# Kernel optimization log

Measured on AMD Instinct MI355X. Metric: run time of the kernel, lower is better.

The kernel has to match this reference:

```python
import jax, jax.numpy as jnp
import numpy as np

N, E, F_IN, H, OUT, G = 40000, 640000, 128, 128, 10, 256


def setup_inputs() -> dict:
    key = jax.random.key(0)
    ks = jax.random.split(key, 8)
    x = jax.random.normal(ks[0], (N, F_IN), dtype=jnp.float32)
    edge_index = jax.random.randint(ks[1], (2, E), 0, N, dtype=jnp.int32)
    batch = jnp.sort(jax.random.randint(ks[2], (N,), 0, G, dtype=jnp.int32))
    W1 = jax.random.normal(ks[3], (F_IN, H), dtype=jnp.float32) / np.sqrt(F_IN)
    b1 = jnp.zeros((H,), dtype=jnp.float32)
    W2 = jax.random.normal(ks[4], (H, H), dtype=jnp.float32) / np.sqrt(H)
    b2 = jnp.zeros((H,), dtype=jnp.float32)
    Wfc = jax.random.normal(ks[5], (H, OUT), dtype=jnp.float32) / np.sqrt(H)
    bfc = jnp.zeros((OUT,), dtype=jnp.float32)
    return {"x": x, "edge_index": edge_index, "batch": batch,
            "W1": W1, "b1": b1, "W2": W2, "b2": b2, "Wfc": Wfc, "bfc": bfc}


def _gcn_conv(x, W, b, row, col, num_nodes):
    # x' = D^{-1/2} (A+I) D^{-1/2} (x W) + b   (self-loops already in row/col)
    xw = x @ W                                            # [N, H]
    ones = jnp.ones(row.shape[0], dtype=x.dtype)
    deg = jax.ops.segment_sum(ones, col, num_segments=num_nodes)
    dinv = jnp.where(deg > 0, jax.lax.rsqrt(jnp.maximum(deg, 1.0)), 0.0)
    norm = dinv[row] * dinv[col]                          # [E+N]
    msg = xw[row] * norm[:, None]                         # gather + scale
    return jax.ops.segment_sum(msg, col, num_segments=num_nodes) + b


def reference(x, edge_index, batch, W1, b1, W2, b2, Wfc, bfc):
    num_nodes = x.shape[0]
    loop = jnp.arange(num_nodes, dtype=edge_index.dtype)
    row = jnp.concatenate([edge_index[0], loop])
    col = jnp.concatenate([edge_index[1], loop])

    h = jax.nn.relu(_gcn_conv(x, W1, b1, row, col, num_nodes))
    h = jax.nn.relu(_gcn_conv(h, W2, b2, row, col, num_nodes))

    # global_mean_pool over graph ids
    sums = jax.ops.segment_sum(h, batch, num_segments=G)  # [G, H]
    cnt = jax.ops.segment_sum(jnp.ones(num_nodes, h.dtype), batch, num_segments=G)
    pooled = sums / jnp.maximum(cnt, 1.0)[:, None]

    logits = pooled @ Wfc + bfc                           # [G, OUT]
    return jax.nn.log_softmax(logits, axis=-1)
```

## Files before the change

### kernel.cpp

```cpp
#include <hip/hip_runtime.h>
#include <math.h>

#define H_DIM 128
#define OUT_DIM 10

typedef __attribute__((ext_vector_type(8))) __bf16 bf16x8;
typedef __attribute__((ext_vector_type(8))) unsigned short ushort8;
typedef __attribute__((ext_vector_type(4))) float f32x4;

__device__ inline unsigned short f2bf_rne(float f) {
    unsigned int u = __float_as_uint(f);
    unsigned int r = u + 0x7FFFu + ((u >> 16) & 1u);
    return (unsigned short)(r >> 16);
}
__device__ inline float bf_lo(unsigned int u) { return __uint_as_float(u << 16); }
__device__ inline float bf_hi(unsigned int u) { return __uint_as_float(u & 0xFFFF0000u); }

__global__ __launch_bounds__(256) void prep_kernel(const float* __restrict__ W1,
                                                   const float* __restrict__ W2,
                                                   unsigned short* __restrict__ Wt1Hi,
                                                   unsigned short* __restrict__ Wt1Lo,
                                                   unsigned short* __restrict__ Wt2Hi,
                                                   unsigned short* __restrict__ Wt2Lo,
                                                   const float* __restrict__ X,
                                                   unsigned short* __restrict__ Xhi,
                                                   unsigned short* __restrict__ Xlo,
                                                   int total8, int hb,
                                                   const int* __restrict__ col,
                                                   int* __restrict__ cnt,
                                                   int* __restrict__ rank, int E) {
    if (blockIdx.x < hb) {
        int e = blockIdx.x * 256 + threadIdx.x;
        if (e < E) rank[e] = atomicAdd(&cnt[col[e]], 1);
    } else if (blockIdx.x < hb + 128) {
        int i = (blockIdx.x - hb) * 256 + threadIdx.x;
        const float* src   = (i < 16384) ? W1    : W2;
        unsigned short* dh = (i < 16384) ? Wt1Hi : Wt2Hi;
        unsigned short* dl = (i < 16384) ? Wt1Lo : Wt2Lo;
        int idx = i & 16383;
        int k = idx >> 7, n = idx & 127;
        float v = src[idx];
        unsigned short hbv = f2bf_rne(v);
        float hf = __uint_as_float((unsigned int)hbv << 16);
        unsigned short lb = f2bf_rne(v - hf);
        dh[n * H_DIM + k] = hbv;
        dl[n * H_DIM + k] = lb;
    } else {
        int i = (blockIdx.x - hb - 128) * 256 + threadIdx.x;
        if (i >= total8) return;
        const float* p = X + (size_t)i * 8;
        f32x4 a = *(const f32x4*)p;
        f32x4 b = *(const f32x4*)(p + 4);
        float v[8] = {a.x, a.y, a.z, a.w, b.x, b.y, b.z, b.w};
        ushort8 h, l;
        #pragma unroll
        for (int j = 0; j < 8; ++j) {
            unsigned short hbv = f2bf_rne(v[j]);
            float hf = __uint_as_float((unsigned int)hbv << 16);
            h[j] = hbv;
            l[j] = f2bf_rne(v[j] - hf);
        }
        *(ushort8*)(Xhi + (size_t)i * 8) = h;
        *(ushort8*)(Xlo + (size_t)i * 8) = l;
    }
}

__global__ __launch_bounds__(256) void scan_phase1(const int* __restrict__ cnt,
                                                   int* __restrict__ blockSums,
                                                   float* __restrict__ dinv, int N) {
    __shared__ int red[256];
    int base = blockIdx.x * 1024;
    int t = threadIdx.x;
    int s = 0;
    for (int i = 0; i < 4; ++i) {
        int idx = base + t * 4 + i;
        if (idx < N) {
            int cv = cnt[idx];
            s += cv;
            dinv[idx] = rsqrtf((float)cv + 1.0f);
        }
    }
    red[t] = s;
    __syncthreads();
    for (int d = 128; d > 0; d >>= 1) {
        if (t < d) red[t] += red[t + d];
        __syncthreads();
    }
    if (t == 0) blockSums[blockIdx.x] = red[0];
}

__global__ __launch_bounds__(256) void scan_phase23(const int* __restrict__ cnt,
                                                    const int* __restrict__ blockSums,
                                                    int* __restrict__ offs, int N, int B) {
    __shared__ int red[256];
    __shared__ int bsum[256];
    int base = blockIdx.x * 1024;
    int t = threadIdx.x;

    bsum[t] = (t < B && t < (int)blockIdx.x) ? blockSums[t] : 0;

    int v[4];
    int s = 0;
    for (int i = 0; i < 4; ++i) {
        int idx = base + t * 4 + i;
        v[i] = (idx < N) ? cnt[idx] : 0;
        s += v[i];
    }
    red[t] = s;
    __syncthreads();
    for (int d = 128; d > 0; d >>= 1) {
        if (t < d) bsum[t] += bsum[t + d];
        __syncthreads();
    }
    for (int d = 1; d < 256; d <<= 1) {
        int x = (t >= d) ? red[t - d] : 0;
        __syncthreads();
        red[t] += x;
        __syncthreads();
    }
    int run = bsum[0] + ((t == 0) ? 0 : red[t - 1]);
    for (int i = 0; i < 4; ++i) {
        int idx = base + t * 4 + i;
        if (idx < N) { offs[idx] = run; run += v[i]; }
    }
    if ((int)blockIdx.x == B - 1 && t == 255) offs[N] = run;
}

__global__ __launch_bounds__(256) void scatter_gemm1(
        const int* __restrict__ row, const int* __restrict__ col,
        const int* __restrict__ rank, const float* __restrict__ dinv,
        const int* __restrict__ offs, int2* __restrict__ csr, int E, int sb,
        const unsigned short* __restrict__ Ahi, const unsigned short* __restrict__ Alo,
        const unsigned short* __restrict__ WtHi, const unsigned short* __restrict__ WtLo,
        unsigned short* __restrict__ Yb, int N) {
    if (blockIdx.x < (unsigned)sb) {
        int e = blockIdx.x * 256 + threadIdx.x;
        if (e >= E) return;
        int r = row[e], c = col[e], rk = rank[e];
        int pos = offs[c] + rk;
        int2 p; p.x = r; p.y = __float_as_int(dinv[r] * dinv[c]);
        csr[pos] = p;
        return;
    }
    int blk  = blockIdx.x - sb;
    int lane = threadIdx.x & 63;
    int wv   = threadIdx.x >> 6;
    int m16  = lane & 15;
    int quad = lane >> 4;
    int nodeBase = blk * 32;

    f32x4 acc[2][2] = {};

    #pragma unroll
    for (int kt = 0; kt < 4; ++kt) {
        int k0 = kt * 32 + quad * 8;

        ushort8 aHi[2], aLo[2];
        #pragma unroll
        for (int mi = 0; mi < 2; ++mi) {
            int node = nodeBase + mi * 16 + m16;
            if (node >= N) node = N - 1;
            size_t off = (size_t)node * H_DIM + k0;
            aHi[mi] = *(const ushort8*)(Ahi + off);
            aLo[mi] = *(const ushort8*)(Alo + off);
        }

        ushort8 bHi[2], bLo[2];
        #pragma unroll
        for (int ni = 0; ni < 2; ++ni) {
            int n = (wv * 2 + ni) * 16 + m16;
            size_t off = (size_t)n * H_DIM + k0;
            bHi[ni] = *(const ushort8*)(WtHi + off);
            bLo[ni] = *(const ushort8*)(WtLo + off);
        }

        #pragma unroll
        for (int mi = 0; mi < 2; ++mi)
            #pragma unroll
            for (int ni = 0; ni < 2; ++ni) {
                acc[mi][ni] = __builtin_amdgcn_mfma_f32_16x16x32_bf16(
                    __builtin_bit_cast(bf16x8, aHi[mi]),
                    __builtin_bit_cast(bf16x8, bHi[ni]), acc[mi][ni], 0, 0, 0);
                acc[mi][ni] = __builtin_amdgcn_mfma_f32_16x16x32_bf16(
                    __builtin_bit_cast(bf16x8, aLo[mi]),
                    __builtin_bit_cast(bf16x8, bHi[ni]), acc[mi][ni], 0, 0, 0);
                acc[mi][ni] = __builtin_amdgcn_mfma_f32_16x16x32_bf16(
                    __builtin_bit_cast(bf16x8, aHi[mi]),
                    __builtin_bit_cast(bf16x8, bLo[ni]), acc[mi][ni], 0, 0, 0);
            }
    }

    #pragma unroll
    for (int mi = 0; mi < 2; ++mi)
        #pragma unroll
        for (int r = 0; r < 4; ++r) {
            int node = nodeBase + mi * 16 + quad * 4 + r;
            if (node < N) {
                #pragma unroll
                for (int ni = 0; ni < 2; ++ni) {
                    int c = (wv * 2 + ni) * 16 + m16;
                    Yb[(size_t)node * H_DIM + c] = f2bf_rne(acc[mi][ni][r]);
                }
            }
        }
}

__global__ __launch_bounds__(256) void gemm_mfma_bf16A(const unsigned short* __restrict__ Xb,
                                                       const unsigned short* __restrict__ WtHi,
                                                       const unsigned short* __restrict__ WtLo,
                                                       unsigned short* __restrict__ Yb, int N) {
    int lane = threadIdx.x & 63;
    int wv   = threadIdx.x >> 6;
    int m16  = lane & 15;
    int quad = lane >> 4;
    int nodeBase = blockIdx.x * 32;

    f32x4 acc[2][2] = {};

    #pragma unroll
    for (int kt = 0; kt < 4; ++kt) {
        int k0 = kt * 32 + quad * 8;

        ushort8 a[2];
        #pragma unroll
        for (int mi = 0; mi < 2; ++mi) {
            int node = nodeBase + mi * 16 + m16;
            if (node >= N) node = N - 1;
            a[mi] = *(const ushort8*)(Xb + (size_t)node * H_DIM + k0);
        }

        ushort8 bHi[2], bLo[2];
        #pragma unroll
        for (int ni = 0; ni < 2; ++ni) {
            int n = (wv * 2 + ni) * 16 + m16;
            size_t off = (size_t)n * H_DIM + k0;
            bHi[ni] = *(const ushort8*)(WtHi + off);
            bLo[ni] = *(const ushort8*)(WtLo + off);
        }

        #pragma unroll
        for (int mi = 0; mi < 2; ++mi)
            #pragma unroll
            for (int ni = 0; ni < 2; ++ni) {
                acc[mi][ni] = __builtin_amdgcn_mfma_f32_16x16x32_bf16(
                    __builtin_bit_cast(bf16x8, a[mi]),
                    __builtin_bit_cast(bf16x8, bHi[ni]), acc[mi][ni], 0, 0, 0);
                acc[mi][ni] = __builtin_amdgcn_mfma_f32_16x16x32_bf16(
                    __builtin_bit_cast(bf16x8, a[mi]),
                    __builtin_bit_cast(bf16x8, bLo[ni]), acc[mi][ni], 0, 0, 0);
            }
    }

    #pragma unroll
    for (int mi = 0; mi < 2; ++mi)
        #pragma unroll
        for (int r = 0; r < 4; ++r) {
            int node = nodeBase + mi * 16 + quad * 4 + r;
            if (node < N) {
                #pragma unroll
                for (int ni = 0; ni < 2; ++ni) {
                    int c = (wv * 2 + ni) * 16 + m16;
                    Yb[(size_t)node * H_DIM + c] = f2bf_rne(acc[mi][ni][r]);
                }
            }
        }
}

__global__ __launch_bounds__(256) void agg_fused(const unsigned short* __restrict__ XWb,
                                                 const float* __restrict__ dinv,
                                                 const int2* __restrict__ csr,
                                                 const int* __restrict__ offs,
                                                 const float* __restrict__ bias,
                                                 unsigned short* __restrict__ OUTb, int N) {
    int wave = (blockIdx.x * 256 + threadIdx.x) >> 6;
    int lane = threadIdx.x & 63;
    if (wave >= N) return;
    int c = wave;
    int start = offs[c], end = offs[c + 1];
    float dc = dinv[c];
    const unsigned int* XW32 = (const unsigned int*)XWb;

    float ax0, ay0;
    {
        unsigned int u = XW32[(size_t)c * 64 + lane];
        float s = dc * dc;
        ax0 = bf_lo(u) * s; ay0 = bf_hi(u) * s;
    }
    float ax1 = 0.f, ay1 = 0.f, ax2 = 0.f, ay2 = 0.f, ax3 = 0.f, ay3 = 0.f;

    for (int base = start; base < end; base += 64) {
        int m = end - base; if (m > 64) m = 64;
        int2 ce; ce.x = 0; ce.y = 0;
        if (lane < m) ce = csr[base + lane];

        int j = 0;
        for (; j + 3 < m; j += 4) {
            int r0 = __shfl(ce.x, j);     int b0 = __shfl(ce.y, j);
            int r1 = __shfl(ce.x, j + 1); int b1 = __shfl(ce.y, j + 1);
            int r2 = __shfl(ce.x, j + 2); int b2 = __shfl(ce.y, j + 2);
            int r3 = __shfl(ce.x, j + 3); int b3 = __shfl(ce.y, j + 3);
            unsigned int g0 = XW32[(size_t)r0 * 64 + lane];
            unsigned int g1 = XW32[(size_t)r1 * 64 + lane];
            unsigned int g2 = XW32[(size_t)r2 * 64 + lane];
            unsigned int g3 = XW32[(size_t)r3 * 64 + lane];
            float n0 = __int_as_float(b0);
            float n1 = __int_as_float(b1);
            float n2 = __int_as_float(b2);
            float n3 = __int_as_float(b3);
            ax0 += bf_lo(g0) * n0; ay0 += bf_hi(g0) * n0;
            ax1 += bf_lo(g1) * n1; ay1 += bf_hi(g1) * n1;
            ax2 += bf_lo(g2) * n2; ay2 += bf_hi(g2) * n2;
            ax3 += bf_lo(g3) * n3; ay3 += bf_hi(g3) * n3;
        }
        for (; j < m; ++j) {
            int r = __shfl(ce.x, j); int b = __shfl(ce.y, j);
            unsigned int g = XW32[(size_t)r * 64 + lane];
            float nrm = __int_as_float(b);
            ax1 += bf_lo(g) * nrm; ay1 += bf_hi(g) * nrm;
        }
    }
    float ax = (ax0 + ax1) + (ax2 + ax3);
    float ay = (ay0 + ay1) + (ay2 + ay3);
    float2 b = ((const float2*)bias)[lane];
    ax = fmaxf(ax + b.x, 0.f);
    ay = fmaxf(ay + b.y, 0.f);
    unsigned int o = (unsigned int)f2bf_rne(ax) | ((unsigned int)f2bf_rne(ay) << 16);
    ((unsigned int*)(OUTb + (size_t)c * H_DIM))[lane] = o;
}

__global__ __launch_bounds__(256) void pool_partial(const unsigned short* __restrict__ Hb,
                                                    const int* __restrict__ batch,
                                                    float* __restrict__ pooledSum, int N) {
    __shared__ int sb[64];
    int base = blockIdx.x * 64;
    int t = threadIdx.x;
    if (t < 64) {
        int idx = base + t;
        sb[t] = (idx < N) ? batch[idx] : -1;
    }
    __syncthreads();
    int f   = t & 127;
    int sub = t >> 7;
    int n0  = sub * 32;
    float acc = 0.f;
    int curg = -1;
    #pragma unroll 4
    for (int i = 0; i < 32; ++i) {
        int n = base + n0 + i;
        if (n >= N) break;
        int g = sb[n0 + i];
        if (g != curg) {
            if (curg >= 0) atomicAdd(&pooledSum[curg * H_DIM + f], acc);
            acc = 0.f; curg = g;
        }
        acc += __uint_as_float(((unsigned int)Hb[(size_t)n * H_DIM + f]) << 16);
    }
    if (curg >= 0) atomicAdd(&pooledSum[curg * H_DIM + f], acc);
}

__global__ __launch_bounds__(64) void head_kernel(const float* __restrict__ pooledSum,
                                                  const int* __restrict__ batch,
                                                  const float* __restrict__ Wfc,
                                                  const float* __restrict__ bfc,
                                                  float* __restrict__ out, int N) {
    __shared__ float sl[OUT_DIM + 2];
    __shared__ int bounds[2];
    int g = blockIdx.x;
    int j = threadIdx.x;
    if (j < 2) {
        int v = g + j;
        int lo = 0, hi = N;
        while (lo < hi) {
            int mid = (lo + hi) >> 1;
            if (batch[mid] < v) lo = mid + 1; else hi = mid;
        }
        bounds[j] = lo;
    }
    __syncthreads();
    int cnt = bounds[1] - bounds[0];
    float inv = 1.0f / (float)(cnt > 0 ? cnt : 1);
    if (j < OUT_DIM) {
        float acc = 0.f;
        const float* p = pooledSum + g * H_DIM;
        for (int k = 0; k < H_DIM; ++k) acc += p[k] * Wfc[k * OUT_DIM + j];
        sl[j] = acc * inv + bfc[j];
    }
    __syncthreads();
    if (j == 0) {
        float m = sl[0];
        for (int i = 1; i < OUT_DIM; ++i) m = fmaxf(m, sl[i]);
        float s = 0.f;
        for (int i = 0; i < OUT_DIM; ++i) s += expf(sl[i] - m);
        sl[OUT_DIM] = m + logf(s);
    }
    __syncthreads();
    if (j < OUT_DIM) out[g * OUT_DIM + j] = sl[j] - sl[OUT_DIM];
}

extern "C" void kernel_launch(void* const* d_in, const int* in_sizes, int n_in,
                              void* d_out, int out_size, void* d_ws, size_t ws_size,
                              hipStream_t stream) {
    const float* x     = (const float*)d_in[0];
    const int*   ei    = (const int*)  d_in[1];
    const int*   batch = (const int*)  d_in[2];
    const float* W1    = (const float*)d_in[3];
    const float* b1    = (const float*)d_in[4];
    const float* W2    = (const float*)d_in[5];
    const float* b2    = (const float*)d_in[6];
    const float* Wfc   = (const float*)d_in[7];
    const float* bfc   = (const float*)d_in[8];
    float* out = (float*)d_out;

    int N = in_sizes[2];
    int E = in_sizes[1] / 2;
    int G = out_size / OUT_DIM;
    const int* row = ei;
    const int* col = ei + E;

    char* wsb = (char*)d_ws;
    size_t nAlign = (size_t)((N + 256) / 256) * 256;
    size_t eAlign = (size_t)((E + 255) / 256) * 256;
    int*   cnt       = (int*)wsb;
    float* pooledSum = (float*)(cnt + nAlign);
    int*   offs      = (int*)(pooledSum + (size_t)G * H_DIM);
    int*   rank      = offs + nAlign;
    float* dinv      = (float*)(rank + eAlign);
    int2*  csr       = (int2*)(dinv + nAlign);
    unsigned short* Xb = (unsigned short*)(csr + E);
    unsigned short* Hb = Xb + (size_t)N * H_DIM;
    int* blockSums = (int*)(Hb + (size_t)N * H_DIM);
    unsigned short* Wt1Hi = (unsigned short*)(blockSums + 256);
    unsigned short* Wt1Lo = Wt1Hi + H_DIM * H_DIM;
    unsigned short* Wt2Hi = Wt1Lo + H_DIM * H_DIM;
    unsigned short* Wt2Lo = Wt2Hi + H_DIM * H_DIM;
    unsigned short* Xhi = Wt2Lo + H_DIM * H_DIM;
    unsigned short* Xlo = Xhi + (size_t)N * H_DIM;

    int scanBlocks = (N + 1023) / 1024;
    int total8 = N * H_DIM / 8;
    int xb = (total8 + 255) / 256;
    int histBlocks = (E + 255) / 256;
    int gemmBlocks = (N + 31) / 32;

    hipMemsetAsync(cnt, 0, (nAlign + (size_t)G * H_DIM) * sizeof(int), stream);

    prep_kernel<<<histBlocks + 128 + xb, 256, 0, stream>>>(
        W1, W2, Wt1Hi, Wt1Lo, Wt2Hi, Wt2Lo, x, Xhi, Xlo, total8, histBlocks,
        col, cnt, rank, E);

    scan_phase1<<<scanBlocks, 256, 0, stream>>>(cnt, blockSums, dinv, N);
    scan_phase23<<<scanBlocks, 256, 0, stream>>>(cnt, blockSums, offs, N, scanBlocks);

    scatter_gemm1<<<histBlocks + gemmBlocks, 256, 0, stream>>>(
        row, col, rank, dinv, offs, csr, E, histBlocks,
        Xhi, Xlo, Wt1Hi, Wt1Lo, Xb, N);

    int aggBlocks = (N + 3) / 4;

    agg_fused<<<aggBlocks, 256, 0, stream>>>(Xb, dinv, csr, offs, b1, Hb, N);

    gemm_mfma_bf16A<<<gemmBlocks, 256, 0, stream>>>(Hb, Wt2Hi, Wt2Lo, Xb, N);
    agg_fused<<<aggBlocks, 256, 0, stream>>>(Xb, dinv, csr, offs, b2, Hb, N);

    pool_partial<<<(N + 63) / 64, 256, 0, stream>>>(Hb, batch, pooledSum, N);
    head_kernel<<<G, 64, 0, stream>>>(pooledSum, batch, Wfc, bfc, out, N);
}
```

Before: 249.2 us.

## Fuse X bf16 split into GEMM1 and mean-pool into second aggregation

The input features are no longer pre-split into hi/lo bf16 buffers in the prep kernel. GEMM1 now reads fp32 X directly and does the split in registers, which removes a full write and re-read of two N×128 bf16 arrays. The second aggregation is templated to reduce its four per-wave node outputs in shared memory and atomically add them into the pooled sums, so the separate pool kernel and the Hb write/read are gone. In exchange it adds a block barrier and more atomics (up to four per feature per block) in the aggregation, and GEMM1 reads fp32 with redundant conversions across waves.

```diff
diff --git a/kernel.cpp b/kernel.cpp
--- a/kernel.cpp
+++ b/kernel.cpp
@@ -22,17 +22,14 @@
                                                    unsigned short* __restrict__ Wt1Lo,
                                                    unsigned short* __restrict__ Wt2Hi,
                                                    unsigned short* __restrict__ Wt2Lo,
-                                                   const float* __restrict__ X,
-                                                   unsigned short* __restrict__ Xhi,
-                                                   unsigned short* __restrict__ Xlo,
-                                                   int total8, int hb,
+                                                   int hb,
                                                    const int* __restrict__ col,
                                                    int* __restrict__ cnt,
                                                    int* __restrict__ rank, int E) {
-    if (blockIdx.x < hb) {
+    if (blockIdx.x < (unsigned)hb) {
         int e = blockIdx.x * 256 + threadIdx.x;
         if (e < E) rank[e] = atomicAdd(&cnt[col[e]], 1);
-    } else if (blockIdx.x < hb + 128) {
+    } else {
         int i = (blockIdx.x - hb) * 256 + threadIdx.x;
         const float* src   = (i < 16384) ? W1    : W2;
         unsigned short* dh = (i < 16384) ? Wt1Hi : Wt2Hi;
@@ -45,23 +42,6 @@
         unsigned short lb = f2bf_rne(v - hf);
         dh[n * H_DIM + k] = hbv;
         dl[n * H_DIM + k] = lb;
-    } else {
-        int i = (blockIdx.x - hb - 128) * 256 + threadIdx.x;
-        if (i >= total8) return;
-        const float* p = X + (size_t)i * 8;
-        f32x4 a = *(const f32x4*)p;
-        f32x4 b = *(const f32x4*)(p + 4);
-        float v[8] = {a.x, a.y, a.z, a.w, b.x, b.y, b.z, b.w};
-        ushort8 h, l;
-        #pragma unroll
-        for (int j = 0; j < 8; ++j) {
-            unsigned short hbv = f2bf_rne(v[j]);
-            float hf = __uint_as_float((unsigned int)hbv << 16);
-            h[j] = hbv;
-            l[j] = f2bf_rne(v[j] - hf);
-        }
-        *(ushort8*)(Xhi + (size_t)i * 8) = h;
-        *(ushort8*)(Xlo + (size_t)i * 8) = l;
     }
 }
 
@@ -130,7 +110,7 @@
         const int* __restrict__ row, const int* __restrict__ col,
         const int* __restrict__ rank, const float* __restrict__ dinv,
         const int* __restrict__ offs, int2* __restrict__ csr, int E, int sb,
-        const unsigned short* __restrict__ Ahi, const unsigned short* __restrict__ Alo,
+        const float* __restrict__ Xf,
         const unsigned short* __restrict__ WtHi, const unsigned short* __restrict__ WtLo,
         unsigned short* __restrict__ Yb, int N) {
     if (blockIdx.x < (unsigned)sb) {
@@ -160,9 +140,16 @@
         for (int mi = 0; mi < 2; ++mi) {
             int node = nodeBase + mi * 16 + m16;
             if (node >= N) node = N - 1;
-            size_t off = (size_t)node * H_DIM + k0;
-            aHi[mi] = *(const ushort8*)(Ahi + off);
-            aLo[mi] = *(const ushort8*)(Alo + off);
+            const float* p = Xf + (size_t)node * H_DIM + k0;
+            f32x4 u = *(const f32x4*)p;
+            f32x4 w = *(const f32x4*)(p + 4);
+            float vv[8] = {u.x, u.y, u.z, u.w, w.x, w.y, w.z, w.w};
+            #pragma unroll
+            for (int j = 0; j < 8; ++j) {
+                unsigned short hbv = f2bf_rne(vv[j]);
+                aHi[mi][j] = hbv;
+                aLo[mi][j] = f2bf_rne(vv[j] - __uint_as_float((unsigned int)hbv << 16));
+            }
         }
 
         ushort8 bHi[2], bLo[2];
@@ -266,96 +253,101 @@
         }
 }
 
-__global__ __launch_bounds__(256) void agg_fused(const unsigned short* __restrict__ XWb,
-                                                 const float* __restrict__ dinv,
-                                                 const int2* __restrict__ csr,
-                                                 const int* __restrict__ offs,
-                                                 const float* __restrict__ bias,
-                                                 unsigned short* __restrict__ OUTb, int N) {
+template <int POOL>
+__global__ __launch_bounds__(256) void agg_fused_t(const unsigned short* __restrict__ XWb,
+                                                   const float* __restrict__ dinv,
+                                                   const int2* __restrict__ csr,
+                                                   const int* __restrict__ offs,
+                                                   const float* __restrict__ bias,
+                                                   unsigned short* __restrict__ OUTb,
+                                                   const int* __restrict__ batch,
+                                                   float* __restrict__ pooledSum, int N) {
     int wave = (blockIdx.x * 256 + threadIdx.x) >> 6;
     int lane = threadIdx.x & 63;
-    if (wave >= N) return;
+    int wv   = threadIdx.x >> 6;
+    bool active = wave < N;
+    if (!POOL && !active) return;
+
+    float ax = 0.f, ay = 0.f;
     int c = wave;
-    int start = offs[c], end = offs[c + 1];
-    float dc = dinv[c];
-    const unsigned int* XW32 = (const unsigned int*)XWb;
-
-    float ax0, ay0;
-    {
-        unsigned int u = XW32[(size_t)c * 64 + lane];
-        float s = dc * dc;
-        ax0 = bf_lo(u) * s; ay0 = bf_hi(u) * s;
-    }
-    float ax1 = 0.f, ay1 = 0.f, ax2 = 0.f, ay2 = 0.f, ax3 = 0.f, ay3 = 0.f;
-
-    for (int base = start; base < end; base += 64) {
-        int m = end - base; if (m > 64) m = 64;
-        int2 ce; ce.x = 0; ce.y = 0;
-        if (lane < m) ce = csr[base + lane];
-
-        int j = 0;
-        for (; j + 3 < m; j += 4) {
-            int r0 = __shfl(ce.x, j);     int b0 = __shfl(ce.y, j);
-            int r1 = __shfl(ce.x, j + 1); int b1 = __shfl(ce.y, j + 1);
-            int r2 = __shfl(ce.x, j + 2); int b2 = __shfl(ce.y, j + 2);
-            int r3 = __shfl(ce.x, j + 3); int b3 = __shfl(ce.y, j + 3);
-            unsigned int g0 = XW32[(size_t)r0 * 64 + lane];
-            unsigned int g1 = XW32[(size_t)r1 * 64 + lane];
-            unsigned int g2 = XW32[(size_t)r2 * 64 + lane];
-            unsigned int g3 = XW32[(size_t)r3 * 64 + lane];
-            float n0 = __int_as_float(b0);
-            float n1 = __int_as_float(b1);
-            float n2 = __int_as_float(b2);
-            float n3 = __int_as_float(b3);
-            ax0 += bf_lo(g0) * n0; ay0 += bf_hi(g0) * n0;
-            ax1 += bf_lo(g1) * n1; ay1 += bf_hi(g1) * n1;
-            ax2 += bf_lo(g2) * n2; ay2 += bf_hi(g2) * n2;
-            ax3 += bf_lo(g3) * n3; ay3 += bf_hi(g3) * n3;
-        }
-        for (; j < m; ++j) {
-            int r = __shfl(ce.x, j); int b = __shfl(ce.y, j);
-            unsigned int g = XW32[(size_t)r * 64 + lane];
-            float nrm = __int_as_float(b);
-            ax1 += bf_lo(g) * nrm; ay1 += bf_hi(g) * nrm;
-        }
-    }
-    float ax = (ax0 + ax1) + (ax2 + ax3);
-    float ay = (ay0 + ay1) + (ay2 + ay3);
-    float2 b = ((const float2*)bias)[lane];
-    ax = fmaxf(ax + b.x, 0.f);
-    ay = fmaxf(ay + b.y, 0.f);
-    unsigned int o = (unsigned int)f2bf_rne(ax) | ((unsigned int)f2bf_rne(ay) << 16);
-    ((unsigned int*)(OUTb + (size_t)c * H_DIM))[lane] = o;
-}
-
-__global__ __launch_bounds__(256) void pool_partial(const unsigned short* __restrict__ Hb,
-                                                    const int* __restrict__ batch,
-                                                    float* __restrict__ pooledSum, int N) {
-    __shared__ int sb[64];
-    int base = blockIdx.x * 64;
-    int t = threadIdx.x;
-    if (t < 64) {
-        int idx = base + t;
-        sb[t] = (idx < N) ? batch[idx] : -1;
-    }
-    __syncthreads();
-    int f   = t & 127;
-    int sub = t >> 7;
-    int n0  = sub * 32;
-    float acc = 0.f;
-    int curg = -1;
-    #pragma unroll 4
-    for (int i = 0; i < 32; ++i) {
-        int n = base + n0 + i;
-        if (n >= N) break;
-        int g = sb[n0 + i];
-        if (g != curg) {
-            if (curg >= 0) atomicAdd(&pooledSum[curg * H_DIM + f], acc);
-            acc = 0.f; curg = g;
-        }
-        acc += __uint_as_float(((unsigned int)Hb[(size_t)n * H_DIM + f]) << 16);
-    }
-    if (curg >= 0) atomicAdd(&pooledSum[curg * H_DIM + f], acc);
+    if (active) {
+        int start = offs[c], end = offs[c + 1];
+        float dc = dinv[c];
+        const unsigned int* XW32 = (const unsigned int*)XWb;
+
+        float ax0, ay0;
+        {
+            unsigned int u = XW32[(size_t)c * 64 + lane];
+            float s = dc * dc;
+            ax0 = bf_lo(u) * s; ay0 = bf_hi(u) * s;
+        }
+        float ax1 = 0.f, ay1 = 0.f, ax2 = 0.f, ay2 = 0.f, ax3 = 0.f, ay3 = 0.f;
+
+        for (int base = start; base < end; base += 64) {
+            int m = end - base; if (m > 64) m = 64;
+            int2 ce; ce.x = 0; ce.y = 0;
+            if (lane < m) ce = csr[base + lane];
+
+            int j = 0;
+            for (; j + 3 < m; j += 4) {
+                int r0 = __shfl(ce.x, j);     int b0 = __shfl(ce.y, j);
+                int r1 = __shfl(ce.x, j + 1); int b1 = __shfl(ce.y, j + 1);
+                int r2 = __shfl(ce.x, j + 2); int b2 = __shfl(ce.y, j + 2);
+                int r3 = __shfl(ce.x, j + 3); int b3 = __shfl(ce.y, j + 3);
+                unsigned int g0 = XW32[(size_t)r0 * 64 + lane];
+                unsigned int g1 = XW32[(size_t)r1 * 64 + lane];
+                unsigned int g2 = XW32[(size_t)r2 * 64 + lane];
+                unsigned int g3 = XW32[(size_t)r3 * 64 + lane];
+                float n0 = __int_as_float(b0);
+                float n1 = __int_as_float(b1);
+                float n2 = __int_as_float(b2);
+                float n3 = __int_as_float(b3);
+                ax0 += bf_lo(g0) * n0; ay0 += bf_hi(g0) * n0;
+                ax1 += bf_lo(g1) * n1; ay1 += bf_hi(g1) * n1;
+                ax2 += bf_lo(g2) * n2; ay2 += bf_hi(g2) * n2;
+                ax3 += bf_lo(g3) * n3; ay3 += bf_hi(g3) * n3;
+            }
+            for (; j < m; ++j) {
+                int r = __shfl(ce.x, j); int b = __shfl(ce.y, j);
+                unsigned int g = XW32[(size_t)r * 64 + lane];
+                float nrm = __int_as_float(b);
+                ax1 += bf_lo(g) * nrm; ay1 += bf_hi(g) * nrm;
+            }
+        }
+        ax = (ax0 + ax1) + (ax2 + ax3);
+        ay = (ay0 + ay1) + (ay2 + ay3);
+        float2 b = ((const float2*)bias)[lane];
+        ax = fmaxf(ax + b.x, 0.f);
+        ay = fmaxf(ay + b.y, 0.f);
+    }
+
+    if constexpr (!POOL) {
+        unsigned int o = (unsigned int)f2bf_rne(ax) | ((unsigned int)f2bf_rne(ay) << 16);
+        ((unsigned int*)(OUTb + (size_t)c * H_DIM))[lane] = o;
+        return;
+    } else {
+        __shared__ float lacc[4][H_DIM];
+        __shared__ int lg[4];
+        if (lane == 0) lg[wv] = active ? batch[c] : -1;
+        float2 t2; t2.x = ax; t2.y = ay;
+        ((float2*)(&lacc[wv][0]))[lane] = t2;
+        __syncthreads();
+        int t = threadIdx.x;
+        if (t < H_DIM) {
+            float s = 0.f; int cur = -1;
+            #pragma unroll
+            for (int w = 0; w < 4; ++w) {
+                int g = lg[w];
+                if (g < 0) continue;
+                if (g != cur) {
+                    if (cur >= 0) atomicAdd(&pooledSum[cur * H_DIM + t], s);
+                    s = 0.f; cur = g;
+                }
+                s += lacc[w][t];
+            }
+            if (cur >= 0) atomicAdd(&pooledSum[cur * H_DIM + t], s);
+        }
+    }
 }
 
 __global__ __launch_bounds__(64) void head_kernel(const float* __restrict__ pooledSum,
@@ -433,35 +425,32 @@
     unsigned short* Wt1Lo = Wt1Hi + H_DIM * H_DIM;
     unsigned short* Wt2Hi = Wt1Lo + H_DIM * H_DIM;
     unsigned short* Wt2Lo = Wt2Hi + H_DIM * H_DIM;
-    unsigned short* Xhi = Wt2Lo + H_DIM * H_DIM;
-    unsigned short* Xlo = Xhi + (size_t)N * H_DIM;
 
     int scanBlocks = (N + 1023) / 1024;
-    int total8 = N * H_DIM / 8;
-    int xb = (total8 + 255) / 256;
     int histBlocks = (E + 255) / 256;
     int gemmBlocks = (N + 31) / 32;
 
     hipMemsetAsync(cnt, 0, (nAlign + (size_t)G * H_DIM) * sizeof(int), stream);
 
-    prep_kernel<<<histBlocks + 128 + xb, 256, 0, stream>>>(
-        W1, W2, Wt1Hi, Wt1Lo, Wt2Hi, Wt2Lo, x, Xhi, Xlo, total8, histBlocks,
-        col, cnt, rank, E);
+    prep_kernel<<<histBlocks + 128, 256, 0, stream>>>(
+        W1, W2, Wt1Hi, Wt1Lo, Wt2Hi, Wt2Lo, histBlocks, col, cnt, rank, E);
 
     scan_phase1<<<scanBlocks, 256, 0, stream>>>(cnt, blockSums, dinv, N);
     scan_phase23<<<scanBlocks, 256, 0, stream>>>(cnt, blockSums, offs, N, scanBlocks);
 
     scatter_gemm1<<<histBlocks + gemmBlocks, 256, 0, stream>>>(
         row, col, rank, dinv, offs, csr, E, histBlocks,
-        Xhi, Xlo, Wt1Hi, Wt1Lo, Xb, N);
+        x, Wt1Hi, Wt1Lo, Xb, N);
 
     int aggBlocks = (N + 3) / 4;
 
-    agg_fused<<<aggBlocks, 256, 0, stream>>>(Xb, dinv, csr, offs, b1, Hb, N);
+    agg_fused_t<0><<<aggBlocks, 256, 0, stream>>>(Xb, dinv, csr, offs, b1, Hb,
+                                                  nullptr, nullptr, N);
 
     gemm_mfma_bf16A<<<gemmBlocks, 256, 0, stream>>>(Hb, Wt2Hi, Wt2Lo, Xb, N);
-    agg_fused<<<aggBlocks, 256, 0, stream>>>(Xb, dinv, csr, offs, b2, Hb, N);
-
-    pool_partial<<<(N + 63) / 64, 256, 0, stream>>>(Hb, batch, pooledSum, N);
+
+    agg_fused_t<1><<<aggBlocks, 256, 0, stream>>>(Xb, dinv, csr, offs, b2, nullptr,
+                                                  batch, pooledSum, N);
+
     head_kernel<<<G, 64, 0, stream>>>(pooledSum, batch, Wfc, bfc, out, N);
 }
```

Result: faster. 230.3 us (-7.6%).
